# Kernel tuning notes

Measured on AMD Instinct MI355X. Metric: run time of the kernel, lower is better.

Reference implementation:

```python
import jax, jax.numpy as jnp
import numpy as np

B, T, K = 1024, 512, 48
NEG = -10000.0
START, STOP = K - 2, K - 1


def setup_inputs() -> dict:
    key = jax.random.key(0)
    k1, k2, k3 = jax.random.split(key, 3)
    feats = jax.random.normal(k1, (B, T, K), dtype=jnp.float32)
    transitions = jax.random.normal(k2, (K, K), dtype=jnp.float32) * 0.1
    tags = jax.random.randint(k3, (B, T), 0, K - 2)
    return {"feats": feats, "transitions": transitions, "tags": tags}


def _mask_trans(transitions):
    # transitions[next, prev]; never transition INTO START, never OUT of STOP
    t = transitions.at[START, :].set(NEG)
    t = t.at[:, STOP].set(NEG)
    return t


def _forward_alg(feats, trans):
    # feats: [T, K] -> log partition (scalar)
    Kt = feats.shape[-1]
    init = jnp.full((Kt,), NEG, dtype=feats.dtype).at[START].set(0.0)

    def step(alpha, emit):
        # alpha[prev] + trans[next, prev] -> LSE over prev, add emit[next]
        alpha_new = emit + jax.nn.logsumexp(alpha[None, :] + trans, axis=1)
        return alpha_new, None

    alpha, _ = jax.lax.scan(step, init, feats)
    return jax.nn.logsumexp(alpha + trans[STOP])


def _gold_score(feats, trans, tags):
    # feats: [T, K], tags: [T]
    Tt = tags.shape[0]
    prev = jnp.concatenate([jnp.array([START], dtype=tags.dtype), tags[:-1]])
    emit = feats[jnp.arange(Tt), tags].sum()
    tr = trans[tags, prev].sum()
    return emit + tr + trans[STOP, tags[-1]]


def _viterbi(feats, trans):
    Kt = feats.shape[-1]
    init = jnp.full((Kt,), NEG, dtype=feats.dtype).at[START].set(0.0)

    def step(v, emit):
        scores = v[None, :] + trans           # [next, prev]
        bp = jnp.argmax(scores, axis=1)       # best prev for each next
        v_new = jnp.max(scores, axis=1) + emit
        return v_new, bp

    v, bps = jax.lax.scan(step, init, feats)  # bps: [T, K]
    term = v + trans[STOP]
    best_last = jnp.argmax(term)
    path_score = term[best_last]

    def back(tag, bp):
        return bp[tag], tag

    _, path = jax.lax.scan(back, best_last, bps, reverse=True)
    return path_score, path.astype(jnp.int32)


def reference(feats, transitions, tags):
    trans = _mask_trans(transitions)
    logZ = jax.vmap(lambda f: _forward_alg(f, trans))(feats)            # [B]
    gold = jax.vmap(lambda f, t: _gold_score(f, trans, t))(feats, tags)  # [B]
    nll = logZ - gold                                                    # [B]
    path_score, paths = jax.vmap(lambda f: _viterbi(f, trans))(feats)    # [B], [B,T]
    return nll, path_score, paths
```

## Files before the change

### kernel.cpp

```cpp
#include <hip/hip_runtime.h>
#include <math.h>

#define KS 48
#define TLEN 512
#define BN 1024
#define START_S 46
#define STOP_S 47
#define NEGV -10000.0f
#define PF 8

typedef float v2f __attribute__((ext_vector_type(2)));

__device__ __forceinline__ float bcast_lane0(float v) {
    return __builtin_bit_cast(float, __builtin_amdgcn_readfirstlane(__builtin_bit_cast(int, v)));
}
__device__ __forceinline__ float rlane(float v, int k) {
    return __builtin_bit_cast(float, __builtin_amdgcn_readlane(__builtin_bit_cast(int, v), k));
}

__device__ __forceinline__ void wargmax(float& bv, int& bi) {
    #pragma unroll
    for (int off = 32; off; off >>= 1) {
        float ov = __shfl_xor(bv, off, 64);
        int   oi = __shfl_xor(bi, off, 64);
        if (ov > bv || (ov == bv && oi < bi)) { bv = ov; bi = oi; }
    }
}

__global__ __launch_bounds__(64) void crf8(
    const float* __restrict__ feats,
    const float* __restrict__ trans,
    const int*   __restrict__ tags,
    float*       __restrict__ out,
    float*       __restrict__ vws)
{
    const int lane = threadIdx.x;
    const bool act = lane < KS;

    __shared__ float xbuf[64];
    __shared__ float trans_sh[KS * KS];
    __shared__ unsigned char path_sh[TLEN];

    if (blockIdx.x < BN) {
        const int b = blockIdx.x;
        const float* fb = feats + (size_t)b * TLEN * KS;
        const int*   tb = tags + (size_t)b * TLEN;

        float Erow[KS];
        {
            const float* tr = trans + (act ? lane : 0) * KS;
            #pragma unroll
            for (int p = 0; p < KS; ++p) {
                float tv = act ? tr[p] : NEGV;
                if (lane == START_S) tv = NEGV;
                if (p == STOP_S)     tv = NEGV;
                Erow[p] = __expf(tv);
            }
        }
        float tstart = act ? trans[lane * KS + START_S] : NEGV;
        if (lane == START_S) tstart = NEGV;

        float alpha = (act ? fb[lane] : -INFINITY) + tstart;

        auto fstep = [&](float emv) {
            float s  = bcast_lane0(alpha);
            float ue = __expf(alpha - s);
            xbuf[lane] = ue;
            const float4* uu = (const float4*)xbuf;
            v2f acc0 = {0.f, 0.f}, acc1 = {0.f, 0.f};
            #pragma unroll
            for (int g = 0; g < KS / 4; ++g) {
                float4 u = uu[g];
                v2f ua = {u.x, u.y}, ub = {u.z, u.w};
                v2f ea = {Erow[4 * g + 0], Erow[4 * g + 1]};
                v2f eb = {Erow[4 * g + 2], Erow[4 * g + 3]};
                acc0 = __builtin_elementwise_fma(ua, ea, acc0);
                acc1 = __builtin_elementwise_fma(ub, eb, acc1);
            }
            alpha = emv + s + __logf((acc0.x + acc0.y) + (acc1.x + acc1.y));
        };

        float em[PF];
        #pragma unroll
        for (int j = 0; j < PF; ++j)
            em[j] = act ? fb[(1 + j) * KS + lane] : -INFINITY;
        for (int c = 0; c < 63; ++c) {
            const int t0 = 1 + c * PF;
            float em_n[PF];
            #pragma unroll
            for (int j = 0; j < PF; ++j) {
                int tf = t0 + PF + j;
                em_n[j] = (act && tf < TLEN) ? fb[tf * KS + lane] : -INFINITY;
            }
            #pragma unroll
            for (int j = 0; j < PF; ++j) fstep(em[j]);
            #pragma unroll
            for (int j = 0; j < PF; ++j) em[j] = em_n[j];
        }
        #pragma unroll
        for (int j = 0; j < 7; ++j) fstep(em[j]);

        float tstop = act ? trans[STOP_S * KS + lane] : NEGV;
        if (lane == STOP_S) tstop = NEGV;
        float z = alpha + tstop;
        float mz = z;
        #pragma unroll
        for (int off = 32; off; off >>= 1)
            mz = fmaxf(mz, __shfl_xor(mz, off, 64));
        float se = __expf(z - mz);
        #pragma unroll
        for (int off = 32; off; off >>= 1)
            se += __shfl_xor(se, off, 64);
        float logZ = mz + __logf(se);

        float g = 0.0f;
        for (int t = lane; t < TLEN; t += 64) {
            int tg = tb[t];
            int pg = (t == 0) ? START_S : tb[t - 1];
            g += fb[t * KS + tg] + trans[tg * KS + pg];
        }
        #pragma unroll
        for (int off = 32; off; off >>= 1)
            g += __shfl_xor(g, off, 64);
        g += trans[STOP_S * KS + tb[TLEN - 1]];

        if (lane == 0) out[b] = logZ - g;
    } else {
        const int b = blockIdx.x - BN;
        const float* fb = feats + (size_t)b * TLEN * KS;
        float* vw = vws + (size_t)b * TLEN * KS;

        float Trow[KS];
        {
            const float* tr = trans + (act ? lane : 0) * KS;
            #pragma unroll
            for (int p = 0; p < KS; ++p) {
                float tv = act ? tr[p] : NEGV;
                if (lane == START_S) tv = NEGV;
                if (p == STOP_S)     tv = NEGV;
                Trow[p] = tv;
            }
        }

        float vit = (lane == START_S) ? 0.0f : NEGV;

        auto vstep = [&](float emv, int t) {
            xbuf[lane] = vit;
            const float4* ww = (const float4*)xbuf;
            v2f m0 = {-3.0e38f, -3.0e38f}, m1 = {-3.0e38f, -3.0e38f};
            #pragma unroll
            for (int g = 0; g < KS / 4; ++g) {
                float4 w = ww[g];
                v2f wa = {w.x, w.y}, wb = {w.z, w.w};
                v2f ta = {Trow[4 * g + 0], Trow[4 * g + 1]};
                v2f tc = {Trow[4 * g + 2], Trow[4 * g + 3]};
                m0 = __builtin_elementwise_max(m0, wa + ta);
                m1 = __builtin_elementwise_max(m1, wb + tc);
            }
            v2f mm = __builtin_elementwise_max(m0, m1);
            float B = fmaxf(mm.x, mm.y);
            if (act) vw[t * KS + lane] = B;
            vit = B + emv;
        };

        float em[PF];
        #pragma unroll
        for (int j = 0; j < PF; ++j)
            em[j] = act ? fb[j * KS + lane] : 0.0f;
        for (int c = 0; c < 64; ++c) {
            const int t0 = c * PF;
            float em_n[PF];
            if (c < 63) {
                #pragma unroll
                for (int j = 0; j < PF; ++j)
                    em_n[j] = act ? fb[(t0 + PF + j) * KS + lane] : 0.0f;
            }
            #pragma unroll
            for (int j = 0; j < PF; ++j) vstep(em[j], t0 + j);
            if (c < 63) {
                #pragma unroll
                for (int j = 0; j < PF; ++j) em[j] = em_n[j];
            }
        }

        for (int idx = lane; idx < KS * KS; idx += 64) {
            int n = idx / KS, p = idx - n * KS;
            float tv = trans[idx];
            if (n == START_S) tv = NEGV;
            if (p == STOP_S)  tv = NEGV;
            trans_sh[idx] = tv;
        }

        float tstop = act ? trans[STOP_S * KS + lane] : NEGV;
        if (lane == STOP_S) tstop = NEGV;

        float Bcur = act ? vw[(TLEN - 1) * KS + lane] : 0.0f;
        float ecur = act ? fb[(TLEN - 1) * KS + lane] : 0.0f;
        float vlast = Bcur + ecur;
        float bv = act ? (vlast + tstop) : -3.0e38f;
        int   bidx = act ? lane : 9999;
        wargmax(bv, bidx);
        int tag = __builtin_amdgcn_readfirstlane(bidx);
        if (lane == 0) {
            out[BN + b] = bv;
            path_sh[TLEN - 1] = (unsigned char)tag;
        }

        float Bp[4], Ep[4];
        #pragma unroll
        for (int j = 0; j < 4; ++j) {
            int r = TLEN - 2 - j;
            Bp[j] = act ? vw[r * KS + lane] : 0.0f;
            Ep[j] = act ? fb[r * KS + lane] : 0.0f;
        }
        #pragma unroll 4
        for (int s = 0; s <= TLEN - 2; ++s) {
            const int slot = s & 3;
            float Bv = Bp[slot], Ev = Ep[slot];
            int nr = TLEN - 6 - s;
            if (nr >= 0) {
                Bp[slot] = act ? vw[nr * KS + lane] : 0.0f;
                Ep[slot] = act ? fb[nr * KS + lane] : 0.0f;
            }
            float v  = Bv + Ev;
            float tr = trans_sh[tag * KS + lane];
            float sc = act ? (v + tr) : -INFINITY;
            float bt = rlane(Bcur, tag);
            unsigned long long mk =
                __ballot(sc == bt) & ((1ULL << KS) - 1ULL);
            tag = __builtin_amdgcn_readfirstlane((int)__builtin_ctzll(mk));
            if (lane == 0) path_sh[TLEN - 2 - s] = (unsigned char)tag;
            Bcur = Bv;
        }

        __syncthreads();
        float* pout = out + 2 * BN + (size_t)b * TLEN;
        for (int t = lane; t < TLEN; t += 64)
            pout[t] = (float)path_sh[t];
    }
}

__global__ __launch_bounds__(64) void crf_split4(
    const float* __restrict__ feats, const float* __restrict__ trans,
    const int* __restrict__ tags, float* __restrict__ out,
    unsigned char* __restrict__ bp_g)
{
    const int lane = threadIdx.x;
    const bool act = lane < KS;

    __shared__ float buf[2][64];
    __shared__ unsigned char path_sh[TLEN];
    __shared__ __align__(16) unsigned char seg[64 * KS];

    if (blockIdx.x < BN) {
        const int b = blockIdx.x;
        const float* fb = feats + (size_t)b * TLEN * KS;
        const int*   tb = tags + (size_t)b * TLEN;

        float Erow[KS];
        {
            const float* tr = trans + (act ? lane : 0) * KS;
            #pragma unroll
            for (int p = 0; p < KS; ++p) {
                float tv = act ? tr[p] : NEGV;
                if (lane == START_S) tv = NEGV;
                if (p == STOP_S)     tv = NEGV;
                Erow[p] = __expf(tv);
            }
        }
        float tstart = act ? trans[lane * KS + START_S] : NEGV;
        if (lane == START_S) tstart = NEGV;

        float alpha = (act ? fb[lane] : -INFINITY) + tstart;

        auto fstep = [&](float emv, int t) {
            float s  = bcast_lane0(alpha);
            float ue = __expf(alpha - s);
            const int bsel = t & 1;
            buf[bsel][lane] = ue;
            __syncthreads();
            const float4* uu = (const float4*)buf[bsel];
            v2f acc0 = {0.f, 0.f}, acc1 = {0.f, 0.f};
            #pragma unroll
            for (int g = 0; g < KS / 4; ++g) {
                float4 u = uu[g];
                v2f ua = {u.x, u.y}, ub = {u.z, u.w};
                v2f ea = {Erow[4 * g + 0], Erow[4 * g + 1]};
                v2f eb = {Erow[4 * g + 2], Erow[4 * g + 3]};
                acc0 = __builtin_elementwise_fma(ua, ea, acc0);
                acc1 = __builtin_elementwise_fma(ub, eb, acc1);
            }
            alpha = emv + s + __logf((acc0.x + acc0.y) + (acc1.x + acc1.y));
        };

        float em[PF];
        #pragma unroll
        for (int j = 0; j < PF; ++j)
            em[j] = act ? fb[(1 + j) * KS + lane] : -INFINITY;
        for (int c = 0; c < 63; ++c) {
            const int t0 = 1 + c * PF;
            float em_n[PF];
            #pragma unroll
            for (int j = 0; j < PF; ++j) {
                int tf = t0 + PF + j;
                em_n[j] = (act && tf < TLEN) ? fb[tf * KS + lane] : -INFINITY;
            }
            #pragma unroll
            for (int j = 0; j < PF; ++j) fstep(em[j], t0 + j);
            #pragma unroll
            for (int j = 0; j < PF; ++j) em[j] = em_n[j];
        }
        #pragma unroll
        for (int j = 0; j < 7; ++j) fstep(em[j], 505 + j);

        float tstop = act ? trans[STOP_S * KS + lane] : NEGV;
        if (lane == STOP_S) tstop = NEGV;
        float z = alpha + tstop;
        float mz = z;
        #pragma unroll
        for (int off = 32; off; off >>= 1)
            mz = fmaxf(mz, __shfl_xor(mz, off, 64));
        float se = __expf(z - mz);
        #pragma unroll
        for (int off = 32; off; off >>= 1)
            se += __shfl_xor(se, off, 64);
        float logZ = mz + __logf(se);

        float g = 0.0f;
        for (int t = lane; t < TLEN; t += 64) {
            int tg = tb[t];
            int pg = (t == 0) ? START_S : tb[t - 1];
            g += fb[t * KS + tg] + trans[tg * KS + pg];
        }
        #pragma unroll
        for (int off = 32; off; off >>= 1)
            g += __shfl_xor(g, off, 64);
        g += trans[STOP_S * KS + tb[TLEN - 1]];

        if (lane == 0) out[b] = logZ - g;
    } else {
        const int b = blockIdx.x - BN;
        const float* fb = feats + (size_t)b * TLEN * KS;
        unsigned char* bpb = bp_g + (size_t)b * TLEN * KS;

        float Trow[KS];
        {
            const float* tr = trans + (act ? lane : 0) * KS;
            #pragma unroll
            for (int p = 0; p < KS; ++p) {
                float tv = act ? tr[p] : NEGV;
                if (lane == START_S) tv = NEGV;
                if (p == STOP_S)     tv = NEGV;
                Trow[p] = tv;
            }
        }

        float vit = (lane == START_S) ? 0.0f : NEGV;

        auto vstep = [&](float emv, int t) {
            const int bsel = t & 1;
            buf[bsel][lane] = vit;
            __syncthreads();
            const float4* ww = (const float4*)buf[bsel];
            float bs[12]; int ib[12];
            #pragma unroll
            for (int g = 0; g < KS / 4; ++g) {
                float4 w = ww[g];
                v2f wa = {w.x, w.y}, wb = {w.z, w.w};
                v2f ta = {Trow[4 * g + 0], Trow[4 * g + 1]};
                v2f tc = {Trow[4 * g + 2], Trow[4 * g + 3]};
                v2f sa = wa + ta;
                v2f sb = wb + tc;
                float m01 = fmaxf(sa.x, sa.y); int i01 = (sa.y > sa.x) ? 4 * g + 1 : 4 * g + 0;
                float m23 = fmaxf(sb.x, sb.y); int i23 = (sb.y > sb.x) ? 4 * g + 3 : 4 * g + 2;
                bs[g] = fmaxf(m01, m23);       ib[g] = (m23 > m01) ? i23 : i01;
            }
            #pragma unroll
            for (int st = 0; st < 6; ++st) {
                float a = bs[2 * st], c2 = bs[2 * st + 1];
                int ia = ib[2 * st], ic = ib[2 * st + 1];
                bs[st] = fmaxf(a, c2); ib[st] = (c2 > a) ? ic : ia;
            }
            #pragma unroll
            for (int st = 0; st < 3; ++st) {
                float a = bs[2 * st], c2 = bs[2 * st + 1];
                int ia = ib[2 * st], ic = ib[2 * st + 1];
                bs[st] = fmaxf(a, c2); ib[st] = (c2 > a) ? ic : ia;
            }
            float best = fmaxf(bs[0], bs[1]);
            int   bi   = (bs[1] > bs[0]) ? ib[1] : ib[0];
            bi   = (bs[2] > best) ? ib[2] : bi;
            best = fmaxf(best, bs[2]);
            if (act) bpb[t * KS + lane] = (unsigned char)bi;
            vit = best + emv;
        };

        float em[PF];
        #pragma unroll
        for (int j = 0; j < PF; ++j)
            em[j] = act ? fb[j * KS + lane] : 0.0f;
        for (int c = 0; c < 64; ++c) {
            const int t0 = c * PF;
            float em_n[PF];
            if (c < 63) {
                #pragma unroll
                for (int j = 0; j < PF; ++j)
                    em_n[j] = act ? fb[(t0 + PF + j) * KS + lane] : 0.0f;
            }
            #pragma unroll
            for (int j = 0; j < PF; ++j) vstep(em[j], t0 + j);
            if (c < 63) {
                #pragma unroll
                for (int j = 0; j < PF; ++j) em[j] = em_n[j];
            }
        }

        float tstop = act ? trans[STOP_S * KS + lane] : NEGV;
        if (lane == STOP_S) tstop = NEGV;
        float term = act ? (vit + tstop) : -3.0e38f;
        float bv = term;
        int   bidx = act ? lane : 9999;
        wargmax(bv, bidx);
        if (lane == 0) out[BN + b] = bv;

        int tag = bidx;
        for (int s = 7; s >= 0; --s) {
            const float4* src = (const float4*)(bpb + s * 64 * KS);
            float4* dst = (float4*)seg;
            #pragma unroll
            for (int i = 0; i < 3; ++i)
                dst[lane + 64 * i] = src[lane + 64 * i];
            __syncthreads();
            for (int t = 63; t >= 0; --t) {
                path_sh[s * 64 + t] = (unsigned char)tag;
                tag = seg[t * KS + tag];
            }
            __syncthreads();
        }
        float* pout = out + 2 * BN + (size_t)b * TLEN;
        for (int t = lane; t < TLEN; t += 64)
            pout[t] = (float)path_sh[t];
    }
}

extern "C" void kernel_launch(void* const* d_in, const int* in_sizes, int n_in,
                              void* d_out, int out_size, void* d_ws, size_t ws_size,
                              hipStream_t stream) {
    const float* feats = (const float*)d_in[0];
    const float* trans = (const float*)d_in[1];
    const int*   tags  = (const int*)d_in[2];
    float*       out   = (float*)d_out;
    (void)in_sizes; (void)n_in; (void)out_size;

    const size_t needV = (size_t)BN * TLEN * KS * sizeof(float);
    const size_t needB = (size_t)BN * TLEN * KS;
    if (ws_size >= needV) {
        crf8<<<dim3(2 * BN), dim3(64), 0, stream>>>(feats, trans, tags, out,
                                                    (float*)d_ws);
    } else if (ws_size >= needB) {
        crf_split4<<<dim3(2 * BN), dim3(64), 0, stream>>>(feats, trans, tags, out,
                                                          (unsigned char*)d_ws);
    } else {
        crf_split4<<<dim3(2 * BN), dim3(64), 0, stream>>>(feats, trans, tags, out,
                                                          (unsigned char*)d_ws);
    }
}
```

Before: 441.9 us.

## Replace LDS broadcast with readlane in CRF forward and Viterbi steps

The forward and Viterbi recurrence steps now broadcast each lane's value with v_readlane to scalar registers instead of writing to and reading back from an LDS buffer. This removes an LDS round trip and its wait on the serial per-timestep critical path, at the cost of 48 readlane ops per step. The backtrace prefetch ring grows from 4 to 8 entries, and the last Viterbi row is kept in registers rather than reread from global memory. An explicit vmcnt(0) wait is added before the backtrace so the workspace stores have completed.

```diff
diff --git a/kernel.cpp b/kernel.cpp
--- a/kernel.cpp
+++ b/kernel.cpp
@@ -8,6 +8,7 @@
 #define STOP_S 47
 #define NEGV -10000.0f
 #define PF 8
+#define RING 8
 
 typedef float v2f __attribute__((ext_vector_type(2)));
 
@@ -27,7 +28,7 @@
     }
 }
 
-__global__ __launch_bounds__(64) void crf8(
+__global__ __launch_bounds__(64) void crf9(
     const float* __restrict__ feats,
     const float* __restrict__ trans,
     const int*   __restrict__ tags,
@@ -37,7 +38,6 @@
     const int lane = threadIdx.x;
     const bool act = lane < KS;
 
-    __shared__ float xbuf[64];
     __shared__ float trans_sh[KS * KS];
     __shared__ unsigned char path_sh[TLEN];
 
@@ -65,19 +65,19 @@
         auto fstep = [&](float emv) {
             float s  = bcast_lane0(alpha);
             float ue = __expf(alpha - s);
-            xbuf[lane] = ue;
-            const float4* uu = (const float4*)xbuf;
-            v2f acc0 = {0.f, 0.f}, acc1 = {0.f, 0.f};
+            float a0 = 0.f, a1 = 0.f, a2 = 0.f, a3 = 0.f;
             #pragma unroll
             for (int g = 0; g < KS / 4; ++g) {
-                float4 u = uu[g];
-                v2f ua = {u.x, u.y}, ub = {u.z, u.w};
-                v2f ea = {Erow[4 * g + 0], Erow[4 * g + 1]};
-                v2f eb = {Erow[4 * g + 2], Erow[4 * g + 3]};
-                acc0 = __builtin_elementwise_fma(ua, ea, acc0);
-                acc1 = __builtin_elementwise_fma(ub, eb, acc1);
-            }
-            alpha = emv + s + __logf((acc0.x + acc0.y) + (acc1.x + acc1.y));
+                float u0 = rlane(ue, 4 * g + 0);
+                float u1 = rlane(ue, 4 * g + 1);
+                float u2 = rlane(ue, 4 * g + 2);
+                float u3 = rlane(ue, 4 * g + 3);
+                a0 = __builtin_fmaf(u0, Erow[4 * g + 0], a0);
+                a1 = __builtin_fmaf(u1, Erow[4 * g + 1], a1);
+                a2 = __builtin_fmaf(u2, Erow[4 * g + 2], a2);
+                a3 = __builtin_fmaf(u3, Erow[4 * g + 3], a3);
+            }
+            alpha = emv + s + __logf((a0 + a1) + (a2 + a3));
         };
 
         float em[PF];
@@ -143,23 +143,22 @@
         }
 
         float vit = (lane == START_S) ? 0.0f : NEGV;
+        float lastB = 0.0f;
 
         auto vstep = [&](float emv, int t) {
-            xbuf[lane] = vit;
-            const float4* ww = (const float4*)xbuf;
-            v2f m0 = {-3.0e38f, -3.0e38f}, m1 = {-3.0e38f, -3.0e38f};
+            float b0 = -3.0e38f, b1 = -3.0e38f;
             #pragma unroll
             for (int g = 0; g < KS / 4; ++g) {
-                float4 w = ww[g];
-                v2f wa = {w.x, w.y}, wb = {w.z, w.w};
-                v2f ta = {Trow[4 * g + 0], Trow[4 * g + 1]};
-                v2f tc = {Trow[4 * g + 2], Trow[4 * g + 3]};
-                m0 = __builtin_elementwise_max(m0, wa + ta);
-                m1 = __builtin_elementwise_max(m1, wb + tc);
-            }
-            v2f mm = __builtin_elementwise_max(m0, m1);
-            float B = fmaxf(mm.x, mm.y);
+                float w0 = rlane(vit, 4 * g + 0) + Trow[4 * g + 0];
+                float w1 = rlane(vit, 4 * g + 1) + Trow[4 * g + 1];
+                float w2 = rlane(vit, 4 * g + 2) + Trow[4 * g + 2];
+                float w3 = rlane(vit, 4 * g + 3) + Trow[4 * g + 3];
+                b0 = fmaxf(fmaxf(b0, w0), w1);
+                b1 = fmaxf(fmaxf(b1, w2), w3);
+            }
+            float B = fmaxf(b0, b1);
             if (act) vw[t * KS + lane] = B;
+            lastB = B;
             vit = B + emv;
         };
 
@@ -183,6 +182,8 @@
             }
         }
 
+        asm volatile("s_waitcnt vmcnt(0)" ::: "memory");
+
         for (int idx = lane; idx < KS * KS; idx += 64) {
             int n = idx / KS, p = idx - n * KS;
             float tv = trans[idx];
@@ -194,8 +195,8 @@
         float tstop = act ? trans[STOP_S * KS + lane] : NEGV;
         if (lane == STOP_S) tstop = NEGV;
 
-        float Bcur = act ? vw[(TLEN - 1) * KS + lane] : 0.0f;
-        float ecur = act ? fb[(TLEN - 1) * KS + lane] : 0.0f;
+        float Bcur = lastB;
+        float ecur = em[PF - 1];
         float vlast = Bcur + ecur;
         float bv = act ? (vlast + tstop) : -3.0e38f;
         int   bidx = act ? lane : 9999;
@@ -206,18 +207,18 @@
             path_sh[TLEN - 1] = (unsigned char)tag;
         }
 
-        float Bp[4], Ep[4];
-        #pragma unroll
-        for (int j = 0; j < 4; ++j) {
+        float Bp[RING], Ep[RING];
+        #pragma unroll
+        for (int j = 0; j < RING; ++j) {
             int r = TLEN - 2 - j;
             Bp[j] = act ? vw[r * KS + lane] : 0.0f;
             Ep[j] = act ? fb[r * KS + lane] : 0.0f;
         }
-        #pragma unroll 4
-        for (int s = 0; s <= TLEN - 2; ++s) {
-            const int slot = s & 3;
+
+        auto btstep = [&](int s) {
+            const int slot = s & (RING - 1);
             float Bv = Bp[slot], Ev = Ep[slot];
-            int nr = TLEN - 6 - s;
+            int nr = TLEN - 2 - RING - s;
             if (nr >= 0) {
                 Bp[slot] = act ? vw[nr * KS + lane] : 0.0f;
                 Ep[slot] = act ? fb[nr * KS + lane] : 0.0f;
@@ -231,7 +232,11 @@
             tag = __builtin_amdgcn_readfirstlane((int)__builtin_ctzll(mk));
             if (lane == 0) path_sh[TLEN - 2 - s] = (unsigned char)tag;
             Bcur = Bv;
-        }
+        };
+        #pragma unroll 8
+        for (int s = 0; s < 504; ++s) btstep(s);
+        #pragma unroll
+        for (int s = 504; s <= TLEN - 2; ++s) btstep(s);
 
         __syncthreads();
         float* pout = out + 2 * BN + (size_t)b * TLEN;
@@ -455,7 +460,7 @@
     const size_t needV = (size_t)BN * TLEN * KS * sizeof(float);
     const size_t needB = (size_t)BN * TLEN * KS;
     if (ws_size >= needV) {
-        crf8<<<dim3(2 * BN), dim3(64), 0, stream>>>(feats, trans, tags, out,
+        crf9<<<dim3(2 * BN), dim3(64), 0, stream>>>(feats, trans, tags, out,
                                                     (float*)d_ws);
     } else if (ws_size >= needB) {
         crf_split4<<<dim3(2 * BN), dim3(64), 0, stream>>>(feats, trans, tags, out,
```

New measurement: 476.9 us. 1.08x slower.

## Store byte backpointers in Viterbi instead of float scores and recomputing backtrace

Applied to the files above, without the earlier changes.

The Viterbi half of the kernel now records an argmax index per step as a byte backpointer in global workspace, replacing the float max-score array that the backtrace used to re-derive the best predecessor by comparing recomputed scores. This cuts workspace traffic fourfold and makes the backtrace a simple table walk through shared-memory segments, at the cost of a heavier forward step that tracks indices. The forward step also drops the double-buffered shared buffer and per-step barrier of the old split kernel, relying on a single-wave block. A vmcnt wait is added before the backtrace so the backpointer stores are complete.

```diff
diff --git a/kernel.cpp b/kernel.cpp
--- a/kernel.cpp
+++ b/kernel.cpp
@@ -14,9 +14,6 @@
 __device__ __forceinline__ float bcast_lane0(float v) {
     return __builtin_bit_cast(float, __builtin_amdgcn_readfirstlane(__builtin_bit_cast(int, v)));
 }
-__device__ __forceinline__ float rlane(float v, int k) {
-    return __builtin_bit_cast(float, __builtin_amdgcn_readlane(__builtin_bit_cast(int, v), k));
-}
 
 __device__ __forceinline__ void wargmax(float& bv, int& bi) {
     #pragma unroll
@@ -27,18 +24,18 @@
     }
 }
 
-__global__ __launch_bounds__(64) void crf8(
+__global__ __launch_bounds__(64) void crf10(
     const float* __restrict__ feats,
     const float* __restrict__ trans,
     const int*   __restrict__ tags,
     float*       __restrict__ out,
-    float*       __restrict__ vws)
+    unsigned char* __restrict__ bp_g)
 {
     const int lane = threadIdx.x;
     const bool act = lane < KS;
 
     __shared__ float xbuf[64];
-    __shared__ float trans_sh[KS * KS];
+    __shared__ __align__(16) unsigned char seg[64 * KS];
     __shared__ unsigned char path_sh[TLEN];
 
     if (blockIdx.x < BN) {
@@ -128,7 +125,7 @@
     } else {
         const int b = blockIdx.x - BN;
         const float* fb = feats + (size_t)b * TLEN * KS;
-        float* vw = vws + (size_t)b * TLEN * KS;
+        unsigned char* bpb = bp_g + (size_t)b * TLEN * KS;
 
         float Trow[KS];
         {
@@ -147,221 +144,6 @@
         auto vstep = [&](float emv, int t) {
             xbuf[lane] = vit;
             const float4* ww = (const float4*)xbuf;
-            v2f m0 = {-3.0e38f, -3.0e38f}, m1 = {-3.0e38f, -3.0e38f};
-            #pragma unroll
-            for (int g = 0; g < KS / 4; ++g) {
-                float4 w = ww[g];
-                v2f wa = {w.x, w.y}, wb = {w.z, w.w};
-                v2f ta = {Trow[4 * g + 0], Trow[4 * g + 1]};
-                v2f tc = {Trow[4 * g + 2], Trow[4 * g + 3]};
-                m0 = __builtin_elementwise_max(m0, wa + ta);
-                m1 = __builtin_elementwise_max(m1, wb + tc);
-            }
-            v2f mm = __builtin_elementwise_max(m0, m1);
-            float B = fmaxf(mm.x, mm.y);
-            if (act) vw[t * KS + lane] = B;
-            vit = B + emv;
-        };
-
-        float em[PF];
-        #pragma unroll
-        for (int j = 0; j < PF; ++j)
-            em[j] = act ? fb[j * KS + lane] : 0.0f;
-        for (int c = 0; c < 64; ++c) {
-            const int t0 = c * PF;
-            float em_n[PF];
-            if (c < 63) {
-                #pragma unroll
-                for (int j = 0; j < PF; ++j)
-                    em_n[j] = act ? fb[(t0 + PF + j) * KS + lane] : 0.0f;
-            }
-            #pragma unroll
-            for (int j = 0; j < PF; ++j) vstep(em[j], t0 + j);
-            if (c < 63) {
-                #pragma unroll
-                for (int j = 0; j < PF; ++j) em[j] = em_n[j];
-            }
-        }
-
-        for (int idx = lane; idx < KS * KS; idx += 64) {
-            int n = idx / KS, p = idx - n * KS;
-            float tv = trans[idx];
-            if (n == START_S) tv = NEGV;
-            if (p == STOP_S)  tv = NEGV;
-            trans_sh[idx] = tv;
-        }
-
-        float tstop = act ? trans[STOP_S * KS + lane] : NEGV;
-        if (lane == STOP_S) tstop = NEGV;
-
-        float Bcur = act ? vw[(TLEN - 1) * KS + lane] : 0.0f;
-        float ecur = act ? fb[(TLEN - 1) * KS + lane] : 0.0f;
-        float vlast = Bcur + ecur;
-        float bv = act ? (vlast + tstop) : -3.0e38f;
-        int   bidx = act ? lane : 9999;
-        wargmax(bv, bidx);
-        int tag = __builtin_amdgcn_readfirstlane(bidx);
-        if (lane == 0) {
-            out[BN + b] = bv;
-            path_sh[TLEN - 1] = (unsigned char)tag;
-        }
-
-        float Bp[4], Ep[4];
-        #pragma unroll
-        for (int j = 0; j < 4; ++j) {
-            int r = TLEN - 2 - j;
-            Bp[j] = act ? vw[r * KS + lane] : 0.0f;
-            Ep[j] = act ? fb[r * KS + lane] : 0.0f;
-        }
-        #pragma unroll 4
-        for (int s = 0; s <= TLEN - 2; ++s) {
-            const int slot = s & 3;
-            float Bv = Bp[slot], Ev = Ep[slot];
-            int nr = TLEN - 6 - s;
-            if (nr >= 0) {
-                Bp[slot] = act ? vw[nr * KS + lane] : 0.0f;
-                Ep[slot] = act ? fb[nr * KS + lane] : 0.0f;
-            }
-            float v  = Bv + Ev;
-            float tr = trans_sh[tag * KS + lane];
-            float sc = act ? (v + tr) : -INFINITY;
-            float bt = rlane(Bcur, tag);
-            unsigned long long mk =
-                __ballot(sc == bt) & ((1ULL << KS) - 1ULL);
-            tag = __builtin_amdgcn_readfirstlane((int)__builtin_ctzll(mk));
-            if (lane == 0) path_sh[TLEN - 2 - s] = (unsigned char)tag;
-            Bcur = Bv;
-        }
-
-        __syncthreads();
-        float* pout = out + 2 * BN + (size_t)b * TLEN;
-        for (int t = lane; t < TLEN; t += 64)
-            pout[t] = (float)path_sh[t];
-    }
-}
-
-__global__ __launch_bounds__(64) void crf_split4(
-    const float* __restrict__ feats, const float* __restrict__ trans,
-    const int* __restrict__ tags, float* __restrict__ out,
-    unsigned char* __restrict__ bp_g)
-{
-    const int lane = threadIdx.x;
-    const bool act = lane < KS;
-
-    __shared__ float buf[2][64];
-    __shared__ unsigned char path_sh[TLEN];
-    __shared__ __align__(16) unsigned char seg[64 * KS];
-
-    if (blockIdx.x < BN) {
-        const int b = blockIdx.x;
-        const float* fb = feats + (size_t)b * TLEN * KS;
-        const int*   tb = tags + (size_t)b * TLEN;
-
-        float Erow[KS];
-        {
-            const float* tr = trans + (act ? lane : 0) * KS;
-            #pragma unroll
-            for (int p = 0; p < KS; ++p) {
-                float tv = act ? tr[p] : NEGV;
-                if (lane == START_S) tv = NEGV;
-                if (p == STOP_S)     tv = NEGV;
-                Erow[p] = __expf(tv);
-            }
-        }
-        float tstart = act ? trans[lane * KS + START_S] : NEGV;
-        if (lane == START_S) tstart = NEGV;
-
-        float alpha = (act ? fb[lane] : -INFINITY) + tstart;
-
-        auto fstep = [&](float emv, int t) {
-            float s  = bcast_lane0(alpha);
-            float ue = __expf(alpha - s);
-            const int bsel = t & 1;
-            buf[bsel][lane] = ue;
-            __syncthreads();
-            const float4* uu = (const float4*)buf[bsel];
-            v2f acc0 = {0.f, 0.f}, acc1 = {0.f, 0.f};
-            #pragma unroll
-            for (int g = 0; g < KS / 4; ++g) {
-                float4 u = uu[g];
-                v2f ua = {u.x, u.y}, ub = {u.z, u.w};
-                v2f ea = {Erow[4 * g + 0], Erow[4 * g + 1]};
-                v2f eb = {Erow[4 * g + 2], Erow[4 * g + 3]};
-                acc0 = __builtin_elementwise_fma(ua, ea, acc0);
-                acc1 = __builtin_elementwise_fma(ub, eb, acc1);
-            }
-            alpha = emv + s + __logf((acc0.x + acc0.y) + (acc1.x + acc1.y));
-        };
-
-        float em[PF];
-        #pragma unroll
-        for (int j = 0; j < PF; ++j)
-            em[j] = act ? fb[(1 + j) * KS + lane] : -INFINITY;
-        for (int c = 0; c < 63; ++c) {
-            const int t0 = 1 + c * PF;
-            float em_n[PF];
-            #pragma unroll
-            for (int j = 0; j < PF; ++j) {
-                int tf = t0 + PF + j;
-                em_n[j] = (act && tf < TLEN) ? fb[tf * KS + lane] : -INFINITY;
-            }
-            #pragma unroll
-            for (int j = 0; j < PF; ++j) fstep(em[j], t0 + j);
-            #pragma unroll
-            for (int j = 0; j < PF; ++j) em[j] = em_n[j];
-        }
-        #pragma unroll
-        for (int j = 0; j < 7; ++j) fstep(em[j], 505 + j);
-
-        float tstop = act ? trans[STOP_S * KS + lane] : NEGV;
-        if (lane == STOP_S) tstop = NEGV;
-        float z = alpha + tstop;
-        float mz = z;
-        #pragma unroll
-        for (int off = 32; off; off >>= 1)
-            mz = fmaxf(mz, __shfl_xor(mz, off, 64));
-        float se = __expf(z - mz);
-        #pragma unroll
-        for (int off = 32; off; off >>= 1)
-            se += __shfl_xor(se, off, 64);
-        float logZ = mz + __logf(se);
-
-        float g = 0.0f;
-        for (int t = lane; t < TLEN; t += 64) {
-            int tg = tb[t];
-            int pg = (t == 0) ? START_S : tb[t - 1];
-            g += fb[t * KS + tg] + trans[tg * KS + pg];
-        }
-        #pragma unroll
-        for (int off = 32; off; off >>= 1)
-            g += __shfl_xor(g, off, 64);
-        g += trans[STOP_S * KS + tb[TLEN - 1]];
-
-        if (lane == 0) out[b] = logZ - g;
-    } else {
-        const int b = blockIdx.x - BN;
-        const float* fb = feats + (size_t)b * TLEN * KS;
-        unsigned char* bpb = bp_g + (size_t)b * TLEN * KS;
-
-        float Trow[KS];
-        {
-            const float* tr = trans + (act ? lane : 0) * KS;
-            #pragma unroll
-            for (int p = 0; p < KS; ++p) {
-                float tv = act ? tr[p] : NEGV;
-                if (lane == START_S) tv = NEGV;
-                if (p == STOP_S)     tv = NEGV;
-                Trow[p] = tv;
-            }
-        }
-
-        float vit = (lane == START_S) ? 0.0f : NEGV;
-
-        auto vstep = [&](float emv, int t) {
-            const int bsel = t & 1;
-            buf[bsel][lane] = vit;
-            __syncthreads();
-            const float4* ww = (const float4*)buf[bsel];
             float bs[12]; int ib[12];
             #pragma unroll
             for (int g = 0; g < KS / 4; ++g) {
@@ -415,6 +197,8 @@
             }
         }
 
+        asm volatile("s_waitcnt vmcnt(0)" ::: "memory");
+
         float tstop = act ? trans[STOP_S * KS + lane] : NEGV;
         if (lane == STOP_S) tstop = NEGV;
         float term = act ? (vit + tstop) : -3.0e38f;
@@ -450,18 +234,8 @@
     const float* trans = (const float*)d_in[1];
     const int*   tags  = (const int*)d_in[2];
     float*       out   = (float*)d_out;
-    (void)in_sizes; (void)n_in; (void)out_size;
-
-    const size_t needV = (size_t)BN * TLEN * KS * sizeof(float);
-    const size_t needB = (size_t)BN * TLEN * KS;
-    if (ws_size >= needV) {
-        crf8<<<dim3(2 * BN), dim3(64), 0, stream>>>(feats, trans, tags, out,
-                                                    (float*)d_ws);
-    } else if (ws_size >= needB) {
-        crf_split4<<<dim3(2 * BN), dim3(64), 0, stream>>>(feats, trans, tags, out,
-                                                          (unsigned char*)d_ws);
-    } else {
-        crf_split4<<<dim3(2 * BN), dim3(64), 0, stream>>>(feats, trans, tags, out,
-                                                          (unsigned char*)d_ws);
-    }
-}
+    (void)in_sizes; (void)n_in; (void)out_size; (void)ws_size;
+
+    crf10<<<dim3(2 * BN), dim3(64), 0, stream>>>(feats, trans, tags, out,
+                                                 (unsigned char*)d_ws);
+}
```

Result: no change. 447.2 us (+1.2%).
